# Performance work log

Measured on AMD Instinct MI355X. Metric: run time of the kernel, lower is better.

Reference implementation:

```python
import jax, jax.numpy as jnp
import numpy as np

EMBED = 512

def setup_inputs() -> dict:
    key = jax.random.key(0)
    ks = jax.random.split(key, 8)
    B, N, E = 4, 2048, EMBED
    s = 1.0 / np.sqrt(E)
    return {
        "value": jax.random.normal(ks[0], (B, N, E), jnp.float32),
        "key": jax.random.normal(ks[1], (B, N, E), jnp.float32),
        "query": jax.random.normal(ks[2], (B, N, E), jnp.float32),
        "Wq": jax.random.normal(ks[3], (E, E), jnp.float32) * s,
        "Wk": jax.random.normal(ks[4], (E, E), jnp.float32) * s,
        "Wv": jax.random.normal(ks[5], (E, E), jnp.float32) * s,
        "Wo": jax.random.normal(ks[6], (E, E), jnp.float32) * s,
        "bo": jax.random.normal(ks[7], (E,), jnp.float32) * 0.01,
    }

def reference(value, key, query, Wq, Wk, Wv, Wo, bo):
    E = query.shape[-1]
    q = jnp.einsum('bne,fe->bnf', query, Wq)   # nn.Linear: x @ W.T
    k = jnp.einsum('bne,fe->bnf', key, Wk)
    v = jnp.einsum('bne,fe->bnf', value, Wv)
    energy = jnp.einsum('bqf,bkf->bqk', q, k)  # [B, N, N]
    attn = jax.nn.softmax(energy / jnp.sqrt(jnp.asarray(E, energy.dtype)), axis=-1)
    out = jnp.einsum('bqk,bkf->bqf', attn, v)
    return jnp.einsum('bnf,of->bno', out, Wo) + bo
```

## Files before the change

kernel.cpp:

```cpp
#include <hip/hip_runtime.h>
#include <stdint.h>


typedef __bf16 bf16;
typedef __bf16 bf16x8 __attribute__((ext_vector_type(8)));
typedef float f32x4 __attribute__((ext_vector_type(4)));

#define GLB_AS __attribute__((address_space(1)))
#define LDS_AS __attribute__((address_space(3)))

struct GArgs {
    const bf16* a[3];
    const bf16* b[3];
    long zsa, zsb, zso;
    int lda, ldb, ldo;
    void* out0;
    void* out1;
    const float* bias;
    const float* srow;
    float* Sout;
    float escale;
};

template<int BM, int BN, int NSEG, int KSEG, int EPI, int SWZ>
__global__ __launch_bounds__(256) void gemm_mfma(GArgs g)
{
    constexpr int KT = KSEG / 64;
    constexpr int WM = BM / 2, WN = BN / 2;
    constexpr int FM = WM / 16, FN = WN / 16;
    constexpr int APASS = BM / 32, BPASS = BN / 32;
    constexpr bool REPACK = (EPI == 1 || EPI == 3 || EPI == 4);
    constexpr int RSTR = WN + 8;
    constexpr int SSTAGE = (BM + BN) * 64 * 2;
    constexpr int SREP = REPACK ? 4 * WM * RSTR * 2 : 0;
    constexpr int SBYTES = SSTAGE > SREP ? SSTAGE : SREP;
    __shared__ char smem[SBYTES];
    bf16* As = (bf16*)smem;
    bf16* Bs = As + BM * 64;

    const int tid = threadIdx.x, lane = tid & 63, wave = tid >> 6;
    const int z = blockIdx.z;
    int bx = blockIdx.x, by = blockIdx.y;
    if constexpr (SWZ == 1) {
        const int lin = bx + (by << 4);
        const int gx = lin & 7, s = lin >> 3;
        bx = (gx & 3) * 4 + (s & 3);
        by = (gx >> 2) * 8 + (s >> 2);
    } else if constexpr (SWZ == 2) {
        const int lin = bx + (by << 2);
        const int gx = lin & 7, s = lin >> 3;
        bx = s & 3;
        by = gx * 8 + (s >> 2);
    } else if constexpr (SWZ == 3) {
        const int lin = bx + (by << 3);
        const int gx = lin & 7, s = lin >> 3;
        bx = s & 7;
        by = gx * 2 + (s >> 3);
    }
    const int m0 = by * BM, n0 = bx * BN;
    const int wm = (wave & 1) * WM, wn = (wave >> 1) * WN;
    const int srow = tid >> 3;
    const int scol = ((tid & 7) ^ (srow & 7)) * 8;

    f32x4 acc[FM][FN] = {};

#pragma unroll
    for (int seg = 0; seg < NSEG; ++seg) {
        const bf16* ap = g.a[seg] + (long)z * g.zsa + (long)(m0 + srow) * g.lda + scol;
        const bf16* bp = g.b[seg] + (long)z * g.zsb + (long)(n0 + srow) * g.ldb + scol;
        for (int kt = 0; kt < KT; ++kt) {
            const int k0 = kt * 64;
            __syncthreads();
#pragma unroll
            for (int p = 0; p < APASS; ++p)
                __builtin_amdgcn_global_load_lds(
                    (const GLB_AS uint32_t*)(ap + k0 + (long)p * 32 * g.lda),
                    (LDS_AS uint32_t*)(As + p * 2048 + tid * 8), 16, 0, 0);
#pragma unroll
            for (int p = 0; p < BPASS; ++p)
                __builtin_amdgcn_global_load_lds(
                    (const GLB_AS uint32_t*)(bp + k0 + (long)p * 32 * g.ldb),
                    (LDS_AS uint32_t*)(Bs + p * 2048 + tid * 8), 16, 0, 0);
            __syncthreads();
#pragma unroll
            for (int kk = 0; kk < 2; ++kk) {
                bf16x8 af[FM], bfr[FN];
#pragma unroll
                for (int i = 0; i < FM; ++i) {
                    const int row = wm + i * 16 + (lane & 15);
                    af[i] = *(const bf16x8*)&As[row * 64 + ((kk * 4 + (lane >> 4)) ^ (lane & 7)) * 8];
                }
#pragma unroll
                for (int j = 0; j < FN; ++j) {
                    const int row = wn + j * 16 + (lane & 15);
                    bfr[j] = *(const bf16x8*)&Bs[row * 64 + ((kk * 4 + (lane >> 4)) ^ (lane & 7)) * 8];
                }
#pragma unroll
                for (int i = 0; i < FM; ++i)
#pragma unroll
                    for (int j = 0; j < FN; ++j)
                        acc[i][j] = __builtin_amdgcn_mfma_f32_16x16x32_bf16(af[i], bfr[j], acc[i][j], 0, 0, 0);
            }
        }
    }

    const int col = lane & 15, qd = lane >> 4;

    if constexpr (EPI == 0 || EPI == 2) {
#pragma unroll
        for (int i = 0; i < FM; ++i)
#pragma unroll
            for (int r = 0; r < 4; ++r) {
                const long gm = m0 + wm + i * 16 + qd * 4 + r;
                float rowscale = 1.0f;
                if (EPI == 2) rowscale = 1.0f / g.srow[(long)z * 2048 + gm];
#pragma unroll
                for (int j = 0; j < FN; ++j) {
                    const long gn = n0 + wn + j * 16 + col;
                    const float x = acc[i][j][r];
                    float* o = (float*)g.out0 + (long)z * g.zso;
                    if (EPI == 0) o[gm * g.ldo + gn] = g.bias ? (x + g.bias[gn]) : x;
                    else          o[gm * g.ldo + gn] = fmaf(x, rowscale, g.bias[gn]);
                }
            }
    } else {
        if constexpr (EPI == 4) {
#pragma unroll
            for (int i = 0; i < FM; ++i)
#pragma unroll
                for (int j = 0; j < FN; ++j)
#pragma unroll
                    for (int r = 0; r < 4; ++r)
                        acc[i][j][r] = exp2f(acc[i][j][r] * g.escale);
#pragma unroll
            for (int i = 0; i < FM; ++i)
#pragma unroll
                for (int r = 0; r < 4; ++r) {
                    float s = 0.f;
#pragma unroll
                    for (int j = 0; j < FN; ++j) s += acc[i][j][r];
#pragma unroll
                    for (int off = 1; off < 16; off <<= 1) s += __shfl_xor(s, off, 64);
                    if ((lane & 15) == 0)
                        atomicAdd(g.Sout + (long)z * 2048 + m0 + wm + i * 16 + qd * 4 + r, s);
                }
        }
        __syncthreads();
        bf16* wa = (bf16*)smem + wave * WM * RSTR;
        constexpr int NP = (EPI == 1) ? 2 : 1;
        constexpr int CPR = WN / 8;
        constexpr int RPI = 64 / CPR;
        static_assert(WM % RPI == 0, "repack rows");
#pragma unroll
        for (int pass = 0; pass < NP; ++pass) {
#pragma unroll
            for (int i = 0; i < FM; ++i)
#pragma unroll
                for (int j = 0; j < FN; ++j)
#pragma unroll
                    for (int r = 0; r < 4; ++r) {
                        const float x = acc[i][j][r];
                        bf16 v;
                        if (EPI == 1) {
                            const bf16 h = (bf16)x;
                            v = pass ? (bf16)(x - (float)h) : h;
                        } else {
                            v = (bf16)x;
                        }
                        wa[(i * 16 + qd * 4 + r) * RSTR + j * 16 + col] = v;
                    }
            bf16* outp = ((pass == 0) ? (bf16*)g.out0 : (bf16*)g.out1) + (long)z * g.zso;
#pragma unroll
            for (int t = 0; t < WM / RPI; ++t) {
                const int rr = t * RPI + (lane / CPR);
                const int cc = (lane % CPR) * 8;
                bf16x8 vv = *(const bf16x8*)&wa[rr * RSTR + cc];
                *(bf16x8*)(outp + (long)(m0 + wm + rr) * g.ldo + n0 + wn + cc) = vv;
            }
            if (NP == 2) asm volatile("s_waitcnt lgkmcnt(0)" ::: "memory");
        }
    }
}

struct SplitArgs {
    const float* x[4];
    bf16* h[4];
    bf16* l[4];
    float* S;
    long n;
    int lomask;
};
__global__ __launch_bounds__(256) void split_f32(SplitArgs s)
{
    const int z = blockIdx.z;
    if (s.S && z == 0 && blockIdx.x < 16) {
        const long si = (long)blockIdx.x * 256 + threadIdx.x;
        ((float2*)s.S)[si] = make_float2(0.f, 0.f);
    }
    const long i = ((long)blockIdx.x * 256 + threadIdx.x) * 8;
    if (i >= s.n) return;
    const float* x = s.x[z];
    float4 a = *(const float4*)(x + i);
    float4 b = *(const float4*)(x + i + 4);
    float vv[8] = {a.x, a.y, a.z, a.w, b.x, b.y, b.z, b.w};
    union { bf16 v[8]; bf16x8 v8; } uh, ul;
#pragma unroll
    for (int j = 0; j < 8; ++j) {
        bf16 hh = (bf16)vv[j];
        uh.v[j] = hh;
        ul.v[j] = (bf16)(vv[j] - (float)hh);
    }
    *(bf16x8*)(s.h[z] + i) = uh.v8;
    if (s.lomask & (1 << z)) *(bf16x8*)(s.l[z] + i) = ul.v8;
}

__global__ __launch_bounds__(256) void transpose_split_w(
    const float* __restrict__ W, bf16* __restrict__ Th, bf16* __restrict__ Tl)
{
    __shared__ float t[64][65];
    const int e0 = blockIdx.y * 64, d0 = blockIdx.x * 64;
#pragma unroll 4
    for (int i = 0; i < 16; ++i) {
        int idx = i * 256 + threadIdx.x;
        int r = idx >> 6, c = idx & 63;
        t[r][c] = W[(long)(e0 + r) * 512 + d0 + c];
    }
    __syncthreads();
#pragma unroll
    for (int i = 0; i < 2; ++i) {
        int idx = i * 256 + threadIdx.x;
        int r = idx >> 3, c = (idx & 7) * 8;
        union { bf16 v[8]; bf16x8 v8; } uh, ul;
#pragma unroll
        for (int j = 0; j < 8; ++j) {
            float x = t[c + j][r];
            bf16 hh = (bf16)x;
            uh.v[j] = hh;
            ul.v[j] = (bf16)(x - (float)hh);
        }
        *(bf16x8*)(Th + (long)(d0 + r) * 512 + e0 + c) = uh.v8;
        *(bf16x8*)(Tl + (long)(d0 + r) * 512 + e0 + c) = ul.v8;
    }
}

#define TILE 64
#define BKF 16
#define PADF 4

__global__ __launch_bounds__(256) void gemm_nt(
    const float* __restrict__ A, const float* __restrict__ B,
    float* __restrict__ C, const float* __restrict__ bias,
    int M, int N, int K, float alpha)
{
    __shared__ float As[BKF][TILE + PADF];
    __shared__ float Bs[BKF][TILE + PADF];
    const int tid = threadIdx.x;
    const int m0 = blockIdx.y * TILE;
    const int n0 = blockIdx.x * TILE;
    const int lr = tid >> 2;
    const int lk = (tid & 3) << 2;
    const int tm = (tid >> 4) << 2;
    const int tn = (tid & 15) << 2;

    float acc[4][4] = {};
    const float* ap = A + (long)(m0 + lr) * K + lk;
    const float* bp = B + (long)(n0 + lr) * K + lk;

    for (int k0 = 0; k0 < K; k0 += BKF) {
        float4 av = *(const float4*)(ap + k0);
        float4 bv = *(const float4*)(bp + k0);
        As[lk + 0][lr] = av.x; As[lk + 1][lr] = av.y;
        As[lk + 2][lr] = av.z; As[lk + 3][lr] = av.w;
        Bs[lk + 0][lr] = bv.x; Bs[lk + 1][lr] = bv.y;
        Bs[lk + 2][lr] = bv.z; Bs[lk + 3][lr] = bv.w;
        __syncthreads();
#pragma unroll
        for (int kk = 0; kk < BKF; ++kk) {
            float4 a4 = *(const float4*)&As[kk][tm];
            float4 b4 = *(const float4*)&Bs[kk][tn];
            float aa[4] = {a4.x, a4.y, a4.z, a4.w};
            float bb[4] = {b4.x, b4.y, b4.z, b4.w};
#pragma unroll
            for (int i = 0; i < 4; ++i)
#pragma unroll
                for (int j = 0; j < 4; ++j)
                    acc[i][j] = fmaf(aa[i], bb[j], acc[i][j]);
        }
        __syncthreads();
    }

    float4 b4 = make_float4(0.f, 0.f, 0.f, 0.f);
    if (bias) b4 = *(const float4*)(bias + n0 + tn);
#pragma unroll
    for (int i = 0; i < 4; ++i) {
        float4 o;
        o.x = fmaf(acc[i][0], alpha, b4.x);
        o.y = fmaf(acc[i][1], alpha, b4.y);
        o.z = fmaf(acc[i][2], alpha, b4.z);
        o.w = fmaf(acc[i][3], alpha, b4.w);
        *(float4*)(C + (long)(m0 + tm + i) * N + n0 + tn) = o;
    }
}

__global__ __launch_bounds__(256) void gemm_nn(
    const float* __restrict__ A, const float* __restrict__ B,
    float* __restrict__ C, int M, int N, int K)
{
    __shared__ float As[BKF][TILE + PADF];
    __shared__ float Bs[BKF][TILE + PADF];
    const int tid = threadIdx.x;
    const int m0 = blockIdx.y * TILE;
    const int n0 = blockIdx.x * TILE;
    const int lr = tid >> 2;
    const int lk = (tid & 3) << 2;
    const int bkk = tid >> 4;
    const int bn = (tid & 15) << 2;
    const int tm = (tid >> 4) << 2;
    const int tn = (tid & 15) << 2;

    float acc[4][4] = {};
    const float* ap = A + (long)(m0 + lr) * K + lk;
    const float* bp = B + (long)bkk * N + n0 + bn;

    for (int k0 = 0; k0 < K; k0 += BKF) {
        float4 av = *(const float4*)(ap + k0);
        As[lk + 0][lr] = av.x; As[lk + 1][lr] = av.y;
        As[lk + 2][lr] = av.z; As[lk + 3][lr] = av.w;
        float4 bv = *(const float4*)(bp + (long)k0 * N);
        *(float4*)&Bs[bkk][bn] = bv;
        __syncthreads();
#pragma unroll
        for (int kk = 0; kk < BKF; ++kk) {
            float4 a4 = *(const float4*)&As[kk][tm];
            float4 b4 = *(const float4*)&Bs[kk][tn];
            float aa[4] = {a4.x, a4.y, a4.z, a4.w};
            float bb[4] = {b4.x, b4.y, b4.z, b4.w};
#pragma unroll
            for (int i = 0; i < 4; ++i)
#pragma unroll
                for (int j = 0; j < 4; ++j)
                    acc[i][j] = fmaf(aa[i], bb[j], acc[i][j]);
        }
        __syncthreads();
    }

#pragma unroll
    for (int i = 0; i < 4; ++i) {
        float4 o = make_float4(acc[i][0], acc[i][1], acc[i][2], acc[i][3]);
        *(float4*)(C + (long)(m0 + tm + i) * N + n0 + tn) = o;
    }
}

__global__ __launch_bounds__(256) void softmax2048(float* __restrict__ E)
{
    const float c = 0.04419417382415922f * 1.44269504088896341f;
    float* p = E + (long)blockIdx.x * 2048;
    const int tid = threadIdx.x;
    float4 r0 = *(const float4*)(p + tid * 8);
    float4 r1 = *(const float4*)(p + tid * 8 + 4);
    float x[8] = {r0.x, r0.y, r0.z, r0.w, r1.x, r1.y, r1.z, r1.w};

    float m = x[0];
#pragma unroll
    for (int i = 1; i < 8; ++i) m = fmaxf(m, x[i]);
#pragma unroll
    for (int off = 32; off > 0; off >>= 1) m = fmaxf(m, __shfl_down(m, off, 64));

    __shared__ float red[4];
    const int lane = tid & 63, wid = tid >> 6;
    if (lane == 0) red[wid] = m;
    __syncthreads();
    m = fmaxf(fmaxf(red[0], red[1]), fmaxf(red[2], red[3]));

    float s = 0.f;
#pragma unroll
    for (int i = 0; i < 8; ++i) {
        x[i] = exp2f((x[i] - m) * c);
        s += x[i];
    }
#pragma unroll
    for (int off = 32; off > 0; off >>= 1) s += __shfl_down(s, off, 64);
    __syncthreads();
    if (lane == 0) red[wid] = s;
    __syncthreads();
    s = red[0] + red[1] + red[2] + red[3];
    const float inv = 1.0f / s;

    r0 = make_float4(x[0] * inv, x[1] * inv, x[2] * inv, x[3] * inv);
    r1 = make_float4(x[4] * inv, x[5] * inv, x[6] * inv, x[7] * inv);
    *(float4*)(p + tid * 8) = r0;
    *(float4*)(p + tid * 8 + 4) = r1;
}


extern "C" void kernel_launch(void* const* d_in, const int* in_sizes, int n_in,
                              void* d_out, int out_size, void* d_ws, size_t ws_size,
                              hipStream_t stream)
{
    const int Bb = 4, Nn = 2048, E = 512;
    const int M = Bb * Nn;
    const float* value = (const float*)d_in[0];
    const float* key_  = (const float*)d_in[1];
    const float* query = (const float*)d_in[2];
    const float* Wq = (const float*)d_in[3];
    const float* Wk = (const float*)d_in[4];
    const float* Wv = (const float*)d_in[5];
    const float* Wo = (const float*)d_in[6];
    const float* bo = (const float*)d_in[7];
    float* out = (float*)d_out;

    const long ME = (long)M * E;
    const long NE = (long)Nn * E;
    const long NN = (long)Nn * Nn;
    const long EE = (long)E * E;

    const size_t oWh   = 0;
    const size_t oWoh  = oWh   + 1048576;
    const size_t oWol  = oWoh  + 524288;
    const size_t oWvTh = oWol  + 524288;
    const size_t oWvTl = oWvTh + 524288;
    const size_t oWovh = oWvTl + 524288;
    const size_t oWovl = oWovh + 524288;
    const size_t oInH  = oWovl + 524288;
    const size_t oVL   = oInH  + 25165824;
    const size_t oQK   = oVL   + 8388608;
    const size_t oU    = oQK   + 16777216;
    const size_t oS    = oU    + 33554432;
    const size_t oWV   = oS    + 32768;
    const size_t REQ   = oWV   + 8388608;

    if (ws_size < REQ) {
        float* q  = (float*)d_ws;
        float* k  = q  + ME;
        float* v  = k  + ME;
        float* en = v  + ME;
        float* ao = en + NN;
        const dim3 blk(256, 1, 1);
        gemm_nt<<<dim3(E / TILE, M / TILE, 1), blk, 0, stream>>>(query, Wq, q, nullptr, M, E, E, 1.0f);
        gemm_nt<<<dim3(E / TILE, M / TILE, 1), blk, 0, stream>>>(key_,  Wk, k, nullptr, M, E, E, 1.0f);
        gemm_nt<<<dim3(E / TILE, M / TILE, 1), blk, 0, stream>>>(value, Wv, v, nullptr, M, E, E, 1.0f);
        for (int b = 0; b < Bb; ++b) {
            const float* qb = q + (long)b * NE;
            const float* kb = k + (long)b * NE;
            const float* vb = v + (long)b * NE;
            float* aob = ao + (long)b * NE;
            gemm_nt<<<dim3(Nn / TILE, Nn / TILE, 1), blk, 0, stream>>>(qb, kb, en, nullptr, Nn, Nn, E, 1.0f);
            softmax2048<<<dim3(Nn, 1, 1), blk, 0, stream>>>(en);
            gemm_nn<<<dim3(E / TILE, Nn / TILE, 1), blk, 0, stream>>>(en, vb, aob, Nn, E, Nn);
        }
        gemm_nt<<<dim3(E / TILE, M / TILE, 1), blk, 0, stream>>>(ao, Wo, out, bo, M, E, E, 1.0f);
        return;
    }

    bf16* Wh    = (bf16*)((char*)d_ws + oWh);
    bf16* Woh   = (bf16*)((char*)d_ws + oWoh);
    bf16* Wol   = (bf16*)((char*)d_ws + oWol);
    bf16* WvTh  = (bf16*)((char*)d_ws + oWvTh);
    bf16* WvTl  = (bf16*)((char*)d_ws + oWvTl);
    bf16* Wovh  = (bf16*)((char*)d_ws + oWovh);
    bf16* Wovl  = (bf16*)((char*)d_ws + oWovl);
    bf16* in_h  = (bf16*)((char*)d_ws + oInH);
    bf16* v_l   = (bf16*)((char*)d_ws + oVL);
    bf16* qk_h  = (bf16*)((char*)d_ws + oQK);
    bf16* U     = (bf16*)((char*)d_ws + oU);
    float* S    = (float*)((char*)d_ws + oS);
    bf16* WVh   = (bf16*)((char*)d_ws + oWV);

    {
        SplitArgs s{};
        s.x[0] = query; s.x[1] = key_; s.x[2] = value;
        s.h[0] = in_h; s.h[1] = in_h + ME; s.h[2] = in_h + 2 * ME;
        s.l[2] = v_l;
        s.S = S;
        s.n = ME;
        s.lomask = 0b100;
        split_f32<<<dim3((unsigned)(ME / 2048), 1, 3), 256, 0, stream>>>(s);
    }
    {
        SplitArgs s{};
        s.x[0] = Wq; s.x[1] = Wk; s.x[2] = Wo;
        s.h[0] = Wh; s.h[1] = Wh + EE; s.h[2] = Woh;
        s.l[2] = Wol;
        s.S = nullptr;
        s.n = EE;
        s.lomask = 0b100;
        split_f32<<<dim3((unsigned)(EE / 2048), 1, 3), 256, 0, stream>>>(s);
    }
    transpose_split_w<<<dim3(8, 8, 1), 256, 0, stream>>>(Wv, WvTh, WvTl);

    {
        GArgs g{};
        g.a[0] = Woh;  g.a[1] = Woh;  g.a[2] = Wol;
        g.b[0] = WvTh; g.b[1] = WvTl; g.b[2] = WvTh;
        g.lda = E; g.ldb = E; g.ldo = E;
        g.out0 = Wovh; g.out1 = Wovl;
        gemm_mfma<64, 64, 3, 512, 1, 0><<<dim3(8, 8, 1), 256, 0, stream>>>(g);
    }

    {
        GArgs g{};
        g.a[0] = in_h;
        g.b[0] = Wh;
        g.zsa = ME; g.zsb = EE; g.zso = ME;
        g.lda = E; g.ldb = E; g.ldo = E;
        g.out0 = qk_h;
        gemm_mfma<128, 128, 1, 512, 3, 2><<<dim3(4, 64, 2), 256, 0, stream>>>(g);
    }

    {
        GArgs g{};
        g.a[0] = qk_h;
        g.b[0] = qk_h + ME;
        g.zsa = NE; g.zsb = NE; g.zso = NN;
        g.lda = E; g.ldb = E; g.ldo = Nn;
        g.out0 = U; g.Sout = S;
        g.escale = 0.06375973295152033f;
        gemm_mfma<128, 128, 1, 512, 4, 1><<<dim3(16, 16, 4), 256, 0, stream>>>(g);
    }

    {
        GArgs g{};
        const bf16* vh = in_h + 2 * ME;
        g.a[0] = Wovh; g.a[1] = Wovh; g.a[2] = Wovl;
        g.b[0] = vh;   g.b[1] = v_l;  g.b[2] = vh;
        g.zsa = 0; g.zsb = NE; g.zso = NE;
        g.lda = E; g.ldb = E; g.ldo = Nn;
        g.out0 = WVh;
        gemm_mfma<64, 128, 3, 512, 3, 0><<<dim3(Nn / 128, E / 64, Bb), 256, 0, stream>>>(g);
    }

    {
        GArgs g{};
        g.a[0] = U; g.b[0] = WVh;
        g.zsa = NN; g.zsb = NE; g.zso = NE;
        g.lda = Nn; g.ldb = Nn; g.ldo = E;
        g.out0 = out; g.bias = bo; g.srow = S;
        gemm_mfma<128, 64, 1, 2048, 2, 3><<<dim3(8, 16, 4), 256, 0, stream>>>(g);
    }
}
```

Baseline: 222.2 us.

## Fold Wq and Wk into one matrix and merge preprocessing launches

New measurement: 238.3 us. +7.3%, slower.

```diff
diff --git a/kernel.cpp b/kernel.cpp
--- a/kernel.cpp
+++ b/kernel.cpp
@@ -56,6 +56,11 @@
         const int gx = lin & 7, s = lin >> 3;
         bx = s & 7;
         by = gx * 2 + (s >> 3);
+    } else if constexpr (SWZ == 4) {
+        const int lin = bx + (by << 2);
+        const int gx = lin & 7, s = lin >> 3;
+        bx = s & 3;
+        by = gx * 2 + (s >> 2);
     }
     const int m0 = by * BM, n0 = bx * BN;
     const int wm = (wave & 1) * WM, wn = (wave >> 1) * WN;
@@ -187,7 +192,7 @@
     bf16* h[4];
     bf16* l[4];
     float* S;
-    long n;
+    long n[4];
     int lomask;
 };
 __global__ __launch_bounds__(256) void split_f32(SplitArgs s)
@@ -198,7 +203,7 @@
         ((float2*)s.S)[si] = make_float2(0.f, 0.f);
     }
     const long i = ((long)blockIdx.x * 256 + threadIdx.x) * 8;
-    if (i >= s.n) return;
+    if (i >= s.n[z]) return;
     const float* x = s.x[z];
     float4 a = *(const float4*)(x + i);
     float4 b = *(const float4*)(x + i + 4);
@@ -214,10 +219,18 @@
     if (s.lomask & (1 << z)) *(bf16x8*)(s.l[z] + i) = ul.v8;
 }
 
-__global__ __launch_bounds__(256) void transpose_split_w(
-    const float* __restrict__ W, bf16* __restrict__ Th, bf16* __restrict__ Tl)
+struct TransArgs {
+    const float* x[3];
+    bf16* th[3];
+    bf16* tl[3];
+};
+__global__ __launch_bounds__(256) void transpose_split_w(TransArgs t3)
 {
     __shared__ float t[64][65];
+    const int z = blockIdx.z;
+    const float* W = t3.x[z];
+    bf16* Th = t3.th[z];
+    bf16* Tl = t3.tl[z];
     const int e0 = blockIdx.y * 64, d0 = blockIdx.x * 64;
 #pragma unroll 4
     for (int i = 0; i < 16; ++i) {
@@ -413,21 +426,18 @@
     const long NE = (long)Nn * E;
     const long NN = (long)Nn * Nn;
     const long EE = (long)E * E;
-
-    const size_t oWh   = 0;
-    const size_t oWoh  = oWh   + 1048576;
-    const size_t oWol  = oWoh  + 524288;
-    const size_t oWvTh = oWol  + 524288;
-    const size_t oWvTl = oWvTh + 524288;
-    const size_t oWovh = oWvTl + 524288;
-    const size_t oWovl = oWovh + 524288;
-    const size_t oInH  = oWovl + 524288;
-    const size_t oVL   = oInH  + 25165824;
-    const size_t oQK   = oVL   + 8388608;
-    const size_t oU    = oQK   + 16777216;
-    const size_t oS    = oU    + 33554432;
-    const size_t oWV   = oS    + 32768;
-    const size_t REQ   = oWV   + 8388608;
+    const size_t EE2 = 524288;
+
+    const size_t oWB  = 0;
+    const size_t oQh  = oWB + 12 * EE2;
+    const size_t oKh  = oQh + 8388608;
+    const size_t oVh  = oKh + 8388608;
+    const size_t oVl  = oVh + 8388608;
+    const size_t oT   = oVl + 8388608;
+    const size_t oU   = oT  + 8388608;
+    const size_t oS   = oU  + 33554432;
+    const size_t oWV  = oS  + 32768;
+    const size_t REQ  = oWV + 8388608;
 
     if (ws_size < REQ) {
         float* q  = (float*)d_ws;
@@ -452,89 +462,86 @@
         return;
     }
 
-    bf16* Wh    = (bf16*)((char*)d_ws + oWh);
-    bf16* Woh   = (bf16*)((char*)d_ws + oWoh);
-    bf16* Wol   = (bf16*)((char*)d_ws + oWol);
-    bf16* WvTh  = (bf16*)((char*)d_ws + oWvTh);
-    bf16* WvTl  = (bf16*)((char*)d_ws + oWvTl);
-    bf16* Wovh  = (bf16*)((char*)d_ws + oWovh);
-    bf16* Wovl  = (bf16*)((char*)d_ws + oWovl);
-    bf16* in_h  = (bf16*)((char*)d_ws + oInH);
-    bf16* v_l   = (bf16*)((char*)d_ws + oVL);
-    bf16* qk_h  = (bf16*)((char*)d_ws + oQK);
-    bf16* U     = (bf16*)((char*)d_ws + oU);
-    float* S    = (float*)((char*)d_ws + oS);
-    bf16* WVh   = (bf16*)((char*)d_ws + oWV);
+    char* wb = (char*)d_ws + oWB;
+    bf16* Woh  = (bf16*)(wb + 0 * EE2);
+    bf16* WkTh = (bf16*)(wb + 1 * EE2);
+    bf16* Wol  = (bf16*)(wb + 2 * EE2);
+    bf16* WkTl = (bf16*)(wb + 3 * EE2);
+    bf16* WvTh = (bf16*)(wb + 4 * EE2);
+    bf16* WqTh = (bf16*)(wb + 5 * EE2);
+    bf16* WvTl = (bf16*)(wb + 6 * EE2);
+    bf16* WqTl = (bf16*)(wb + 7 * EE2);
+    bf16* Wovh = (bf16*)(wb + 8 * EE2);
+    bf16* Hh   = (bf16*)(wb + 9 * EE2);
+    bf16* Wovl = (bf16*)(wb + 10 * EE2);
+    bf16* qh   = (bf16*)((char*)d_ws + oQh);
+    bf16* kh   = (bf16*)((char*)d_ws + oKh);
+    bf16* vh   = (bf16*)((char*)d_ws + oVh);
+    bf16* vl   = (bf16*)((char*)d_ws + oVl);
+    bf16* tq   = (bf16*)((char*)d_ws + oT);
+    bf16* U    = (bf16*)((char*)d_ws + oU);
+    float* S   = (float*)((char*)d_ws + oS);
+    bf16* WVh  = (bf16*)((char*)d_ws + oWV);
 
     {
         SplitArgs s{};
-        s.x[0] = query; s.x[1] = key_; s.x[2] = value;
-        s.h[0] = in_h; s.h[1] = in_h + ME; s.h[2] = in_h + 2 * ME;
-        s.l[2] = v_l;
+        s.x[0] = query; s.x[1] = key_; s.x[2] = value; s.x[3] = Wo;
+        s.h[0] = qh; s.h[1] = kh; s.h[2] = vh; s.h[3] = Woh;
+        s.l[2] = vl; s.l[3] = Wol;
         s.S = S;
-        s.n = ME;
-        s.lomask = 0b100;
-        split_f32<<<dim3((unsigned)(ME / 2048), 1, 3), 256, 0, stream>>>(s);
-    }
-    {
-        SplitArgs s{};
-        s.x[0] = Wq; s.x[1] = Wk; s.x[2] = Wo;
-        s.h[0] = Wh; s.h[1] = Wh + EE; s.h[2] = Woh;
-        s.l[2] = Wol;
-        s.S = nullptr;
-        s.n = EE;
-        s.lomask = 0b100;
-        split_f32<<<dim3((unsigned)(EE / 2048), 1, 3), 256, 0, stream>>>(s);
-    }
-    transpose_split_w<<<dim3(8, 8, 1), 256, 0, stream>>>(Wv, WvTh, WvTl);
-
+        s.n[0] = ME; s.n[1] = ME; s.n[2] = ME; s.n[3] = EE;
+        s.lomask = 0b1100;
+        split_f32<<<dim3((unsigned)(ME / 2048), 1, 4), 256, 0, stream>>>(s);
+    }
+    {
+        TransArgs t3{};
+        t3.x[0] = Wv; t3.x[1] = Wq; t3.x[2] = Wk;
+        t3.th[0] = WvTh; t3.th[1] = WqTh; t3.th[2] = WkTh;
+        t3.tl[0] = WvTl; t3.tl[1] = WqTl; t3.tl[2] = WkTl;
+        transpose_split_w<<<dim3(8, 8, 3), 256, 0, stream>>>(t3);
+    }
     {
         GArgs g{};
         g.a[0] = Woh;  g.a[1] = Woh;  g.a[2] = Wol;
         g.b[0] = WvTh; g.b[1] = WvTl; g.b[2] = WvTh;
+        g.zsa = EE; g.zsb = EE; g.zso = EE;
         g.lda = E; g.ldb = E; g.ldo = E;
         g.out0 = Wovh; g.out1 = Wovl;
-        gemm_mfma<64, 64, 3, 512, 1, 0><<<dim3(8, 8, 1), 256, 0, stream>>>(g);
-    }
-
+        gemm_mfma<64, 64, 3, 512, 1, 0><<<dim3(8, 8, 2), 256, 0, stream>>>(g);
+    }
     {
         GArgs g{};
-        g.a[0] = in_h;
-        g.b[0] = Wh;
-        g.zsa = ME; g.zsb = EE; g.zso = ME;
+        g.a[0] = qh;
+        g.b[0] = Hh;
         g.lda = E; g.ldb = E; g.ldo = E;
-        g.out0 = qk_h;
-        gemm_mfma<128, 128, 1, 512, 3, 2><<<dim3(4, 64, 2), 256, 0, stream>>>(g);
-    }
-
+        g.out0 = tq;
+        gemm_mfma<128, 128, 1, 512, 3, 2><<<dim3(4, 64, 1), 256, 0, stream>>>(g);
+    }
     {
         GArgs g{};
-        g.a[0] = qk_h;
-        g.b[0] = qk_h + ME;
+        g.a[0] = tq;
+        g.b[0] = kh;
         g.zsa = NE; g.zsb = NE; g.zso = NN;
         g.lda = E; g.ldb = E; g.ldo = Nn;
         g.out0 = U; g.Sout = S;
         g.escale = 0.06375973295152033f;
         gemm_mfma<128, 128, 1, 512, 4, 1><<<dim3(16, 16, 4), 256, 0, stream>>>(g);
     }
-
     {
         GArgs g{};
-        const bf16* vh = in_h + 2 * ME;
         g.a[0] = Wovh; g.a[1] = Wovh; g.a[2] = Wovl;
-        g.b[0] = vh;   g.b[1] = v_l;  g.b[2] = vh;
+        g.b[0] = vh;   g.b[1] = vl;   g.b[2] = vh;
         g.zsa = 0; g.zsb = NE; g.zso = NE;
         g.lda = E; g.ldb = E; g.ldo = Nn;
         g.out0 = WVh;
-        gemm_mfma<64, 128, 3, 512, 3, 0><<<dim3(Nn / 128, E / 64, Bb), 256, 0, stream>>>(g);
-    }
-
+        gemm_mfma<128, 128, 3, 512, 3, 0><<<dim3(Nn / 128, E / 128, Bb), 256, 0, stream>>>(g);
+    }
     {
         GArgs g{};
         g.a[0] = U; g.b[0] = WVh;
         g.zsa = NN; g.zsb = NE; g.zso = NE;
         g.lda = Nn; g.ldb = Nn; g.ldo = E;
         g.out0 = out; g.bias = bo; g.srow = S;
-        gemm_mfma<128, 64, 1, 2048, 2, 3><<<dim3(8, 16, 4), 256, 0, stream>>>(g);
-    }
-}
+        gemm_mfma<128, 128, 1, 2048, 2, 4><<<dim3(E / 128, Nn / 128, Bb), 256, 0, stream>>>(g);
+    }
+}
```
